# Performance work log

Measured on AMD Instinct MI355X. Metric: run time of the kernel, lower is better.

The kernel has to match this reference:

```python
import jax, jax.numpy as jnp
import numpy as np

H, W = 101, 31
HEADS, DH, FREQ = 8, 64, 64
C_DIM = 256
INNER = HEADS * DH
EPS = 1e-5


def _conv2d(x, w, b):
    # x: (B, Cin, H, W), w: (Cout, Cin, 3, 3) -> SAME padding, stride 1
    y = jax.lax.conv_general_dilated(x, w, (1, 1), 'SAME',
                                     dimension_numbers=('NCHW', 'OIHW', 'NCHW'))
    return y + b[None, :, None, None]


def setup_inputs() -> dict:
    key = jax.random.key(0)
    ks = jax.random.split(key, 8)
    B = 32
    N = H * W  # 3131
    s = 0.02
    x = jax.random.normal(ks[0], (B, N, C_DIM), jnp.float32)
    conv_fx_w = jax.random.normal(ks[1], (INNER, C_DIM, 3, 3), jnp.float32) * s
    conv_fx_b = jnp.zeros((INNER,), jnp.float32)
    conv_x_w = jax.random.normal(ks[2], (INNER, C_DIM, 3, 3), jnp.float32) * s
    conv_x_b = jnp.zeros((INNER,), jnp.float32)
    gate_w = jax.random.normal(ks[3], (FREQ, DH), jnp.float32) * s  # nn.Linear weight (out,in)
    gate_b = jnp.zeros((FREQ,), jnp.float32)
    temperature = jnp.full((1, HEADS, 1, 1), 0.5, jnp.float32)
    ln_gamma = jnp.ones((FREQ, DH), jnp.float32)
    ln_beta = jnp.zeros((FREQ, DH), jnp.float32)
    mlp_w = jax.random.normal(ks[4], (DH, DH), jnp.float32) * s
    out_w = jax.random.normal(ks[5], (C_DIM, INNER), jnp.float32) * s
    out_b = jnp.zeros((C_DIM,), jnp.float32)
    # fixed (non-trainable) spectral basis, L2-normalized per row like F.normalize(dim=-1)
    inver = jax.random.normal(ks[6], (N, FREQ), jnp.float32)
    inver = inver / jnp.linalg.norm(inver, axis=-1, keepdims=True)
    return dict(x=x, conv_fx_w=conv_fx_w, conv_fx_b=conv_fx_b, conv_x_w=conv_x_w,
                conv_x_b=conv_x_b, gate_w=gate_w, gate_b=gate_b,
                temperature=temperature, ln_gamma=ln_gamma, ln_beta=ln_beta,
                mlp_w=mlp_w, out_w=out_w, out_b=out_b, inver=inver)


def reference(x, conv_fx_w, conv_fx_b, conv_x_w, conv_x_b, gate_w, gate_b,
              temperature, ln_gamma, ln_beta, mlp_w, out_w, out_b, inver):
    B, N, C = x.shape
    xi = x.reshape(B, H, W, C).transpose(0, 3, 1, 2)  # (B, C, H, W)

    def proj(w, b):
        y = _conv2d(xi, w, b)                                  # (B, inner, H, W)
        return y.transpose(0, 2, 3, 1).reshape(B, N, HEADS, DH).transpose(0, 2, 1, 3)  # (B,h,N,d)

    fx_mid = proj(conv_fx_w, conv_fx_b)
    x_mid = proj(conv_x_w, conv_x_b)

    temp = jnp.clip(temperature, 0.1, 5.0)                      # (1,h,1,1)
    logits = jnp.einsum('bhnc,gc->bhng', x_mid, gate_w) + gate_b
    gate = jax.nn.softmax(logits / temp, axis=-1)               # (B,h,N,g)
    eigens = gate * inver[None, None]                           # (B,h,N,g)

    spec = jnp.einsum('bhnc,bhng->bhgc', fx_mid, eigens)        # (B,h,g,c)
    # LayerNorm over the trailing (g, c) axes jointly
    mu = spec.mean(axis=(-2, -1), keepdims=True)
    var = spec.var(axis=(-2, -1), keepdims=True)
    spec = (spec - mu) * jax.lax.rsqrt(var + EPS) * ln_gamma + ln_beta

    out_spec = jnp.einsum('bhgi,io->bhgo', spec, mlp_w)
    out_x = jnp.einsum('bhgc,bhng->bhnc', out_spec, eigens)     # (B,h,N,c)
    out_x = out_x.transpose(0, 2, 1, 3).reshape(B, N, HEADS * DH)
    return jnp.einsum('bnd,cd->bnc', out_x, out_w) + out_b      # to_out (dropout is identity)
```

## Files before the change

### kernel.cpp

```cpp
#include <hip/hip_runtime.h>
#include <hip/hip_bf16.h>
#include <stdint.h>

#define HH 101
#define WW 31
#define NN 3131
#define NPAD 3136
#define BB 32
#define NH 8
#define CDIM 256
#define GG 64
#define HP 103
#define WP 33

typedef __attribute__((ext_vector_type(8))) short bf16x8;
typedef __attribute__((ext_vector_type(4))) float f32x4;
typedef __attribute__((ext_vector_type(4))) unsigned short ushort4_t;
typedef __attribute__((ext_vector_type(8))) unsigned short ushort8_t;
typedef __attribute__((ext_vector_type(4))) float float4_t;

static __device__ __forceinline__ unsigned short f2bf(float f) {
  union { float f; uint32_t u; } v; v.f = f;
  uint32_t u = v.u;
  return (unsigned short)((u + 0x7fffu + ((u >> 16) & 1u)) >> 16);
}
static __device__ __forceinline__ float bf2f(unsigned short h) {
  union { uint32_t u; float f; } v; v.u = ((uint32_t)h) << 16;
  return v.f;
}
static __device__ __forceinline__ void gload_lds16(const void* g, void* l) {
  __builtin_amdgcn_global_load_lds((const __attribute__((address_space(1))) void*)g,
                                   (__attribute__((address_space(3))) void*)l, 16, 0, 0);
}
static __device__ __forceinline__ int xcd_swz(int bid, int nwg) {
  int q = nwg >> 3, r = nwg & 7;
  int xcd = bid & 7, pos = bid >> 3;
  int base = (xcd < r) ? xcd * (q + 1) : r * (q + 1) + (xcd - r) * q;
  return base + pos;
}

__global__ void k_pad(const float* __restrict__ x, unsigned short* __restrict__ xpad, int b0) {
  const int xx = blockIdx.x, yy = blockIdx.y, b = blockIdx.z;
  const int t = threadIdx.x;
  ushort4_t o; o.x = 0; o.y = 0; o.z = 0; o.w = 0;
  if (yy >= 1 && yy <= HH && xx >= 1 && xx <= WW) {
    const int n = (yy - 1) * WW + (xx - 1);
    const float4_t v = *(const float4_t*)(x + (((int64_t)(b0 + b) * NN + n) * CDIM + t * 4));
    o.x = f2bf(v.x); o.y = f2bf(v.y); o.z = f2bf(v.z); o.w = f2bf(v.w);
  }
  *(ushort4_t*)(xpad + (((int64_t)b * HP + yy) * WP + xx) * CDIM + t * 4) = o;
}

__global__ void k_wpack(const float* __restrict__ fxw, const float* __restrict__ xw,
                        const float* __restrict__ fxb, const float* __restrict__ xb,
                        const float* __restrict__ gw,
                        unsigned short* __restrict__ Wb, float* __restrict__ bias,
                        unsigned short* __restrict__ gwb) {
  int tid = blockIdx.x * blockDim.x + threadIdx.x;
  const int total = 9 * 1024 * 256;
  if (tid < total) {
    int cin = tid & 255; int rest = tid >> 8; int co = rest & 1023; int t = rest >> 10;
    float v = (co < 512) ? fxw[(int64_t)co * 2304 + cin * 9 + t]
                         : xw[(int64_t)(co - 512) * 2304 + cin * 9 + t];
    Wb[tid] = f2bf(v);
  }
  if (tid < 1024) bias[tid] = (tid < 512) ? fxb[tid] : xb[tid - 512];
  if (tid < 4096) gwb[tid] = f2bf(gw[tid]);
}

__global__ void k_pprep(const float* __restrict__ mlp, const float* __restrict__ outw,
                        unsigned short* __restrict__ Pt) {
  int h = blockIdx.x >> 6, i = blockIdx.x & 63, co = threadIdx.x;
  float a = 0.f;
  for (int c = 0; c < 64; ++c) a += mlp[i * 64 + c] * outw[(int64_t)co * 512 + h * 64 + c];
  Pt[((int64_t)h * 256 + co) * 64 + i] = f2bf(a);
}

__global__ void k_padzero(unsigned short* __restrict__ fxT, unsigned short* __restrict__ xmid,
                          int CB) {
  int tid = blockIdx.x * blockDim.x + threadIdx.x;
  if (tid >= CB * 2560) return;
  {
    int j = tid % 5; int rc = tid / 5;
    fxT[(int64_t)rc * NPAD + NN + j] = 0;
  }
  {
    int d = tid & 63; int rest = tid >> 6;
    int j = rest % 5; int bh = rest / 5;
    xmid[((int64_t)bh * NPAD + NN + j) * 64 + d] = 0;
  }
}

__launch_bounds__(512, 2)
__global__ void k_conv8(const unsigned short* __restrict__ xpad,
                        const unsigned short* __restrict__ Wb,
                        const float* __restrict__ bias,
                        unsigned short* __restrict__ fxT,
                        unsigned short* __restrict__ xmid) {
  extern __shared__ unsigned short lds[];
  const int swz = xcd_swz(blockIdx.x, gridDim.x);
  const int r   = swz % 52;
  const int b   = swz / 52;
  const int bx  = r & 3;
  const int mt  = r >> 2;
  const int tid = threadIdx.x, wid = tid >> 6, lane = tid & 63;
  const int wm = wid & 3, wn = wid >> 2;
  const int arow = lane & 15, col16 = lane >> 4;
  const int n00 = mt * 256, co00 = bx * 256;

  const int srow = wid * 16 + (lane >> 2);
  const int tc   = ((lane & 3) ^ ((lane >> 3) & 3)) * 8;
  int na0 = n00 + srow;        if (na0 >= NN) na0 = NN - 1;
  int na1 = n00 + srow + 128;  if (na1 >= NN) na1 = NN - 1;
  const int y0 = na0 / WW, x0v = na0 % WW;
  const int y1 = na1 / WW, x1v = na1 % WW;
  const unsigned short* aS0 = xpad + ((int64_t)(b * HP + y0) * WP + x0v) * CDIM + tc;
  const unsigned short* aS1 = xpad + ((int64_t)(b * HP + y1) * WP + x1v) * CDIM + tc;
  const unsigned short* bS0 = Wb + (int64_t)(co00 + srow) * CDIM + tc;
  const unsigned short* bS1 = Wb + (int64_t)(co00 + srow + 128) * CDIM + tc;

  const int rdsz = (col16 ^ ((arow >> 1) & 3)) * 8;

  f32x4 acc[4][8] = {};
  bf16x8 a0[4], a1[4], b03[4], b47[4];

#define STAGE_A(s, kk, aoffv)                                        \
  { unsigned short* d = lds + (s) * 32768 + (kk) * 8192 + wid * 512; \
    gload_lds16(aS0 + (aoffv) + (kk) * 32, d);                       \
    gload_lds16(aS1 + (aoffv) + (kk) * 32, d + 4096); }
#define STAGE_B(s, kk, boffv)                                                \
  { unsigned short* d = lds + (s) * 32768 + 16384 + (kk) * 8192 + wid * 512; \
    gload_lds16(bS0 + (boffv) + (kk) * 32, d);                               \
    gload_lds16(bS1 + (boffv) + (kk) * 32, d + 4096); }
#define KOFF(ks, aoffv, boffv)                              \
  { const int tap = (ks) >> 2;                              \
    const int dy = (tap >= 6) + (tap >= 3);                 \
    const int dx = tap - dy * 3;                            \
    const int cb = ((ks) & 3) << 6;                         \
    aoffv = (dy * WP + dx) * CDIM + cb;                     \
    boffv = tap * 262144 + cb; }
#define RD_A(dst, s, kk, mf)                                                             \
  dst = *(const bf16x8*)(lds + (s) * 32768 + (kk) * 8192 +                               \
                         (wm * 64 + (mf) * 16 + arow) * 32 + rdsz);
#define RD_B(dst, s, kk, nf)                                                             \
  dst = *(const bf16x8*)(lds + (s) * 32768 + 16384 + (kk) * 8192 +                       \
                         (wn * 128 + (nf) * 16 + arow) * 32 + rdsz);
#define MFMA16(aset, bset, nbase)                                                        \
  __builtin_amdgcn_s_setprio(1);                                                         \
  _Pragma("unroll")                                                                      \
  for (int mf = 0; mf < 4; ++mf) {                                                       \
    _Pragma("unroll")                                                                    \
    for (int nf = 0; nf < 4; ++nf)                                                       \
      acc[mf][(nbase) + nf] =                                                            \
        __builtin_amdgcn_mfma_f32_16x16x32_bf16(aset[mf], bset[nf], acc[mf][(nbase) + nf], 0, 0, 0); \
  }                                                                                      \
  __builtin_amdgcn_s_setprio(0);

  int aoff0, boff0;
  KOFF(0, aoff0, boff0);
  STAGE_A(0, 0, aoff0); STAGE_B(0, 0, boff0);
  STAGE_A(0, 1, aoff0); STAGE_B(0, 1, boff0);
  asm volatile("s_waitcnt vmcnt(4)" ::: "memory");
  __builtin_amdgcn_s_barrier();
  asm volatile("" ::: "memory");
  #pragma unroll
  for (int i = 0; i < 4; ++i) { RD_A(a0[i], 0, 0, i); }
  #pragma unroll
  for (int i = 0; i < 4; ++i) { RD_B(b03[i], 0, 0, i); }

  #pragma unroll 1
  for (int t = 0; t < 36; ++t) {
    const int cur = t & 1, nxt = cur ^ 1;
    const int tn = (t < 35) ? t + 1 : 35;
    int aoffn, boffn;
    KOFF(tn, aoffn, boffn);

    #pragma unroll
    for (int i = 0; i < 4; ++i) { RD_B(b47[i], cur, 0, 4 + i); }
    STAGE_A(nxt, 0, aoffn);
    asm volatile("s_waitcnt lgkmcnt(4)" ::: "memory");
    __builtin_amdgcn_sched_barrier(0);
    MFMA16(a0, b03, 0);

    STAGE_B(nxt, 0, boffn);
    asm volatile("s_waitcnt vmcnt(4)" ::: "memory");
    __builtin_amdgcn_s_barrier();
    asm volatile("" ::: "memory");
    #pragma unroll
    for (int i = 0; i < 4; ++i) { RD_A(a1[i], cur, 1, i); }
    #pragma unroll
    for (int i = 0; i < 4; ++i) { RD_B(b03[i], cur, 1, i); }
    asm volatile("s_waitcnt lgkmcnt(8)" ::: "memory");
    __builtin_amdgcn_sched_barrier(0);
    MFMA16(a0, b47, 4);

    #pragma unroll
    for (int i = 0; i < 4; ++i) { RD_B(b47[i], cur, 1, 4 + i); }
    STAGE_A(nxt, 1, aoffn);
    asm volatile("s_waitcnt lgkmcnt(4)" ::: "memory");
    __builtin_amdgcn_sched_barrier(0);
    MFMA16(a1, b03, 0);

    STAGE_B(nxt, 1, boffn);
    asm volatile("s_waitcnt vmcnt(4)" ::: "memory");
    __builtin_amdgcn_s_barrier();
    asm volatile("" ::: "memory");
    #pragma unroll
    for (int i = 0; i < 4; ++i) { RD_A(a0[i], nxt, 0, i); }
    #pragma unroll
    for (int i = 0; i < 4; ++i) { RD_B(b03[i], nxt, 0, i); }
    asm volatile("s_waitcnt lgkmcnt(8)" ::: "memory");
    __builtin_amdgcn_sched_barrier(0);
    MFMA16(a1, b47, 4);
  }

  asm volatile("s_waitcnt vmcnt(0) lgkmcnt(0)" ::: "memory");

  const int rowoff = col16 * 4;
  #pragma unroll
  for (int mf = 0; mf < 4; ++mf) {
    const int nr = n00 + wm * 64 + mf * 16 + rowoff;
    #pragma unroll
    for (int nf = 0; nf < 8; ++nf) {
      const int co = co00 + wn * 128 + nf * 16 + arow;
      const float bvs = bias[co];
      const float v0 = acc[mf][nf][0] + bvs;
      const float v1 = acc[mf][nf][1] + bvs;
      const float v2 = acc[mf][nf][2] + bvs;
      const float v3 = acc[mf][nf][3] + bvs;
      if (bx < 2) {
        const int h = co >> 6, c = co & 63;
        unsigned short* dst = fxT + ((int64_t)((b * NH + h) * 64 + c)) * NPAD + nr;
        if (nr + 3 < NN) {
          ushort4_t o; o.x = f2bf(v0); o.y = f2bf(v1); o.z = f2bf(v2); o.w = f2bf(v3);
          *(ushort4_t*)dst = o;
        } else {
          if (nr + 0 < NN) dst[0] = f2bf(v0);
          if (nr + 1 < NN) dst[1] = f2bf(v1);
          if (nr + 2 < NN) dst[2] = f2bf(v2);
          if (nr + 3 < NN) dst[3] = f2bf(v3);
        }
      } else {
        const int h = (co >> 6) & 7, d = co & 63;
        unsigned short* dst = xmid + ((int64_t)(b * NH + h) * NPAD + nr) * 64 + d;
        if (nr + 0 < NN) dst[0] = f2bf(v0);
        if (nr + 1 < NN) dst[64] = f2bf(v1);
        if (nr + 2 < NN) dst[128] = f2bf(v2);
        if (nr + 3 < NN) dst[192] = f2bf(v3);
      }
    }
  }
#undef STAGE_A
#undef STAGE_B
#undef KOFF
#undef RD_A
#undef RD_B
#undef MFMA16
}

__global__ void k_eig(const unsigned short* __restrict__ xmid,
                      const unsigned short* __restrict__ gwb,
                      const float* __restrict__ gateb,
                      const float* __restrict__ temperature,
                      const float* __restrict__ inver,
                      unsigned short* __restrict__ eigT,
                      unsigned short* __restrict__ eigN) {
  __shared__ unsigned short egN[64 * 72];
  __shared__ unsigned short egT[64 * 72];
  const int nt = blockIdx.x, h = blockIdx.y, b = blockIdx.z;
  const int tid = threadIdx.x;
  const int w = tid >> 6, lane = tid & 63;
  const int n0 = nt * 64 + w * 16;
  const int bh = b * NH + h;
  float tv = temperature[h];
  tv = fminf(fmaxf(tv, 0.1f), 5.0f);
  const float itemp = 1.0f / tv;
  const int arow = lane & 15;
  const int koff = (lane >> 4) * 8;
  const unsigned short* aptr = xmid + ((int64_t)bh * NPAD + (n0 + arow)) * 64 + koff;
  bf16x8 a0 = *(const bf16x8*)(aptr);
  bf16x8 a1 = *(const bf16x8*)(aptr + 32);
  f32x4 acc[4] = {};
  #pragma unroll
  for (int ng = 0; ng < 4; ++ng) {
    const unsigned short* bptr = gwb + (ng * 16 + arow) * 64 + koff;
    bf16x8 b0 = *(const bf16x8*)(bptr);
    bf16x8 b1 = *(const bf16x8*)(bptr + 32);
    acc[ng] = __builtin_amdgcn_mfma_f32_16x16x32_bf16(a0, b0, acc[ng], 0, 0, 0);
    acc[ng] = __builtin_amdgcn_mfma_f32_16x16x32_bf16(a1, b1, acc[ng], 0, 0, 0);
  }
  #pragma unroll
  for (int r = 0; r < 4; ++r) {
    const int nl = w * 16 + ((lane >> 4) << 2) + r;
    const int n = nt * 64 + nl;
    float vals[4];
    #pragma unroll
    for (int ng = 0; ng < 4; ++ng) vals[ng] = (acc[ng][r] + gateb[ng * 16 + arow]) * itemp;
    float mx = fmaxf(fmaxf(vals[0], vals[1]), fmaxf(vals[2], vals[3]));
    #pragma unroll
    for (int s = 1; s < 16; s <<= 1) mx = fmaxf(mx, __shfl_xor(mx, s));
    float ex[4]; float sum = 0.f;
    #pragma unroll
    for (int ng = 0; ng < 4; ++ng) { ex[ng] = __expf(vals[ng] - mx); sum += ex[ng]; }
    #pragma unroll
    for (int s = 1; s < 16; s <<= 1) sum += __shfl_xor(sum, s);
    const float inv = 1.0f / sum;
    const bool valid = (n < NN);
    #pragma unroll
    for (int ng = 0; ng < 4; ++ng) {
      const int g = ng * 16 + arow;
      float iv = valid ? inver[(int64_t)n * GG + g] : 0.f;
      unsigned short u = valid ? f2bf(ex[ng] * inv * iv) : (unsigned short)0;
      egN[nl * 72 + g] = u;
      egT[g * 72 + nl] = u;
    }
  }
  __syncthreads();
  const int row = tid >> 2, c0 = (tid & 3) << 4;
  {
    ushort8_t v0 = *(ushort8_t*)&egN[row * 72 + c0];
    ushort8_t v1 = *(ushort8_t*)&egN[row * 72 + c0 + 8];
    unsigned short* dst = eigN + ((int64_t)bh * NPAD + nt * 64 + row) * 64 + c0;
    *(ushort8_t*)dst = v0; *(ushort8_t*)(dst + 8) = v1;
  }
  {
    ushort8_t v0 = *(ushort8_t*)&egT[row * 72 + c0];
    ushort8_t v1 = *(ushort8_t*)&egT[row * 72 + c0 + 8];
    unsigned short* dst = eigT + ((int64_t)(bh * 64 + row)) * NPAD + nt * 64 + c0;
    *(ushort8_t*)dst = v0; *(ushort8_t*)(dst + 8) = v1;
  }
}

__global__ void k_specA(const unsigned short* __restrict__ eigT,
                        const unsigned short* __restrict__ fxT,
                        float* __restrict__ part) {
  const int q = blockIdx.x, bhl = blockIdx.y;
  const int tid = threadIdx.x, w = tid >> 6, lane = tid & 63;
  const int s = q * 4 + w;
  const int ks0 = (98 * s) >> 3, ks1 = (98 * (s + 1)) >> 3;
  const int arow = lane & 15, col16 = lane >> 4;
  const int koff = col16 * 8;
  const unsigned short* eb = eigT + (int64_t)bhl * 64 * NPAD;
  const unsigned short* fb = fxT + (int64_t)bhl * 64 * NPAD;
  f32x4 acc[4][4] = {};
  for (int ks = ks0; ks < ks1; ++ks) {
    const int k0 = ks * 32 + koff;
    bf16x8 av[4], bv[4];
    #pragma unroll
    for (int mg = 0; mg < 4; ++mg) av[mg] = *(const bf16x8*)(eb + (int64_t)(mg * 16 + arow) * NPAD + k0);
    #pragma unroll
    for (int ng = 0; ng < 4; ++ng) bv[ng] = *(const bf16x8*)(fb + (int64_t)(ng * 16 + arow) * NPAD + k0);
    #pragma unroll
    for (int mg = 0; mg < 4; ++mg)
      #pragma unroll
      for (int ng = 0; ng < 4; ++ng)
        acc[mg][ng] = __builtin_amdgcn_mfma_f32_16x16x32_bf16(av[mg], bv[ng], acc[mg][ng], 0, 0, 0);
  }
  float* pb = part + ((int64_t)bhl * 8 + s) * 4096;
  #pragma unroll
  for (int mg = 0; mg < 4; ++mg)
    #pragma unroll
    for (int ng = 0; ng < 4; ++ng)
      #pragma unroll
      for (int r = 0; r < 4; ++r)
        pb[(mg * 16 + col16 * 4 + r) * 64 + ng * 16 + arow] = acc[mg][ng][r];
}

__global__ void k_specB(const float* __restrict__ part,
                        const float* __restrict__ gamma, const float* __restrict__ beta,
                        const unsigned short* __restrict__ Pt,
                        unsigned short* __restrict__ m2t) {
  __shared__ unsigned short specb[64 * 64];
  __shared__ float red[8];
  __shared__ unsigned short mstrip[4 * 64 * 72];
  const int bhl = blockIdx.x;
  const int h = bhl & 7, bl = bhl >> 3;
  const int tid = threadIdx.x, w = tid >> 6, lane = tid & 63;
  const int arow = lane & 15, col16 = lane >> 4;
  const int koff = col16 * 8;
  const float* pb = part + (int64_t)bhl * 8 * 4096;

  float vloc[16];
  float lsum = 0.f, lsq = 0.f;
  #pragma unroll
  for (int idx = 0; idx < 16; ++idx) {
    const int e = tid + idx * 256;
    float v = 0.f;
    #pragma unroll
    for (int s = 0; s < 8; ++s) v += pb[s * 4096 + e];
    vloc[idx] = v; lsum += v; lsq += v * v;
  }
  #pragma unroll
  for (int s = 1; s < 64; s <<= 1) { lsum += __shfl_xor(lsum, s); lsq += __shfl_xor(lsq, s); }
  if (lane == 0) { red[w] = lsum; red[4 + w] = lsq; }
  __syncthreads();
  const float tsum = red[0] + red[1] + red[2] + red[3];
  const float tsq = red[4] + red[5] + red[6] + red[7];
  const float mu = tsum * (1.0f / 4096.0f);
  const float var = tsq * (1.0f / 4096.0f) - mu * mu;
  const float rs = rsqrtf(var + 1e-5f);
  #pragma unroll
  for (int idx = 0; idx < 16; ++idx) {
    const int e = tid + idx * 256;
    const int g = e >> 6, c = e & 63;
    float sv = (vloc[idx] - mu) * rs * gamma[e] + beta[e];
    specb[g * 64 + ((((c >> 3) ^ (g & 7))) << 3) + (c & 7)] = f2bf(sv);
  }
  __syncthreads();

  f32x4 a2[4][4] = {};
  const unsigned short* pth = Pt + ((int64_t)h * 256 + w * 64) * 64;
  #pragma unroll
  for (int kk = 0; kk < 2; ++kk) {
    const int i0 = kk * 32 + koff;
    const int i8 = (i0 >> 3);
    bf16x8 av2[4], bv2[4];
    #pragma unroll
    for (int mg = 0; mg < 4; ++mg) {
      const int g = mg * 16 + arow;
      av2[mg] = *(const bf16x8*)(specb + g * 64 + ((i8 ^ (g & 7)) << 3));
    }
    #pragma unroll
    for (int ng = 0; ng < 4; ++ng)
      bv2[ng] = *(const bf16x8*)(pth + (ng * 16 + arow) * 64 + i0);
    #pragma unroll
    for (int mg = 0; mg < 4; ++mg)
      #pragma unroll
      for (int ng = 0; ng < 4; ++ng)
        a2[mg][ng] = __builtin_amdgcn_mfma_f32_16x16x32_bf16(av2[mg], bv2[ng], a2[mg][ng], 0, 0, 0);
  }
  unsigned short* ms = mstrip + w * (64 * 72);
  #pragma unroll
  for (int mg = 0; mg < 4; ++mg)
    #pragma unroll
    for (int ng = 0; ng < 4; ++ng)
      #pragma unroll
      for (int r = 0; r < 4; ++r)
        ms[(ng * 16 + arow) * 72 + mg * 16 + col16 * 4 + r] = f2bf(a2[mg][ng][r]);
  __syncthreads();
  #pragma unroll
  for (int e0 = 0; e0 < 8; ++e0) {
    const int e = lane + e0 * 64;
    const int row = e >> 3, g8 = e & 7;
    ushort8_t v = *(ushort8_t*)&ms[row * 72 + g8 * 8];
    *(ushort8_t*)(m2t + ((int64_t)(bl * 256 + w * 64 + row)) * 512 + h * 64 + g8 * 8) = v;
  }
}

__launch_bounds__(256)
__global__ void k_out(const unsigned short* __restrict__ eigN,
                      const unsigned short* __restrict__ m2t,
                      const float* __restrict__ outb,
                      float* __restrict__ out, int b0) {
  const int swz = xcd_swz(blockIdx.x, gridDim.x);
  const int ct = swz & 1;
  const int mt = (swz >> 1) % 25;
  const int b  = swz / 50;
  const int w = threadIdx.x >> 6, lane = threadIdx.x & 63;
  const int wm = w >> 1, wn = w & 1;
  const int arow = lane & 15, koff = (lane >> 4) * 8;
  const int co0 = ct * 128 + wn * 64;
  const int n0 = mt * 128 + wm * 64;
  f32x4 acc[4][4] = {};
  const unsigned short* ebase = eigN + (int64_t)b * NH * NPAD * 64;
  const unsigned short* mbase = m2t + (int64_t)b * 256 * 512;
  for (int ks = 0; ks < 16; ++ks) {
    const int hh = ks >> 1;
    const int g0 = (ks & 1) * 32 + koff;
    bf16x8 av[4], bv[4];
    #pragma unroll
    for (int mg = 0; mg < 4; ++mg) {
      int n = n0 + mg * 16 + arow;
      if (n > NPAD - 1) n = NPAD - 1;
      av[mg] = *(const bf16x8*)(ebase + ((int64_t)hh * NPAD + n) * 64 + g0);
    }
    #pragma unroll
    for (int ng = 0; ng < 4; ++ng)
      bv[ng] = *(const bf16x8*)(mbase + (int64_t)(co0 + ng * 16 + arow) * 512 + ks * 32 + koff);
    #pragma unroll
    for (int mg = 0; mg < 4; ++mg)
      #pragma unroll
      for (int ng = 0; ng < 4; ++ng)
        acc[mg][ng] = __builtin_amdgcn_mfma_f32_16x16x32_bf16(av[mg], bv[ng], acc[mg][ng], 0, 0, 0);
  }
  #pragma unroll
  for (int mg = 0; mg < 4; ++mg) {
    const int nr = n0 + mg * 16 + ((lane >> 4) << 2);
    #pragma unroll
    for (int ng = 0; ng < 4; ++ng) {
      const int co = co0 + ng * 16 + arow;
      const float bv = outb[co];
      #pragma unroll
      for (int r = 0; r < 4; ++r) {
        if (nr + r < NN)
          out[((int64_t)(b0 + b) * NN + nr + r) * 256 + co] = acc[mg][ng][r] + bv;
      }
    }
  }
}

extern "C" void kernel_launch(void* const* d_in, const int* in_sizes, int n_in,
                              void* d_out, int out_size, void* d_ws, size_t ws_size,
                              hipStream_t stream) {
  const float* x     = (const float*)d_in[0];
  const float* fxw   = (const float*)d_in[1];
  const float* fxb   = (const float*)d_in[2];
  const float* xw    = (const float*)d_in[3];
  const float* xb    = (const float*)d_in[4];
  const float* gw    = (const float*)d_in[5];
  const float* gb    = (const float*)d_in[6];
  const float* temp  = (const float*)d_in[7];
  const float* gamma = (const float*)d_in[8];
  const float* beta  = (const float*)d_in[9];
  const float* mlp   = (const float*)d_in[10];
  const float* outw  = (const float*)d_in[11];
  const float* outb  = (const float*)d_in[12];
  const float* inver = (const float*)d_in[13];
  float* out = (float*)d_out;
  char* ws = (char*)d_ws;
  (void)in_sizes; (void)n_in; (void)out_size;

  hipFuncSetAttribute(reinterpret_cast<const void*>(k_conv8),
                      hipFuncAttributeMaxDynamicSharedMemorySize, 131072);

  int CB = 1;
  {
    const int cands[5] = {16, 8, 4, 2, 1};
    for (int i = 0; i < 5; ++i) {
      unsigned long long need = 4993024ull + (unsigned long long)cands[i] * 14847488ull;
      if (need <= (unsigned long long)ws_size) { CB = cands[i]; break; }
    }
  }

  unsigned short* Wb   = (unsigned short*)(ws + 0);
  float*          bias = (float*)(ws + 4718592);
  unsigned short* gwb  = (unsigned short*)(ws + 4722688);
  unsigned short* Pt   = (unsigned short*)(ws + 4730880);
  const size_t F0      = 4993024;
  const size_t szXpad  = (size_t)CB * 1740288;
  const size_t szM2t   = (size_t)CB * 262144;
  const size_t szBig   = (size_t)CB * 3211264;
  unsigned short* xpad = (unsigned short*)(ws + F0);
  float*          part = (float*)(ws + F0);
  unsigned short* m2t  = (unsigned short*)(ws + F0 + szXpad);
  unsigned short* fxT  = (unsigned short*)(ws + F0 + szXpad + szM2t);
  unsigned short* xmid = (unsigned short*)(ws + F0 + szXpad + szM2t + szBig);
  unsigned short* eigT = (unsigned short*)(ws + F0 + szXpad + szM2t + 2 * szBig);
  unsigned short* eigN = (unsigned short*)(ws + F0 + szXpad + szM2t + 3 * szBig);

  k_wpack<<<dim3(9216), dim3(256), 0, stream>>>(fxw, xw, fxb, xb, gw, Wb, bias, gwb);
  k_pprep<<<dim3(512), dim3(256), 0, stream>>>(mlp, outw, Pt);

  for (int b0 = 0; b0 < BB; b0 += CB) {
    k_pad<<<dim3(WP, HP, CB), dim3(64), 0, stream>>>(x, xpad, b0);
    k_padzero<<<dim3(CB * 10), dim3(256), 0, stream>>>(fxT, xmid, CB);
    k_conv8<<<dim3(52 * CB), dim3(512), 131072, stream>>>(xpad, Wb, bias, fxT, xmid);
    k_eig<<<dim3(49, 8, CB), dim3(256), 0, stream>>>(xmid, gwb, gb, temp, inver, eigT, eigN);
    k_specA<<<dim3(2, CB * 8), dim3(256), 0, stream>>>(eigT, fxT, part);
    k_specB<<<dim3(CB * 8), dim3(256), 0, stream>>>(part, gamma, beta, Pt, m2t);
    k_out<<<dim3(50 * CB), dim3(256), 0, stream>>>(eigN, m2t, outb, out, b0);
  }
}
```

Baseline: 889.3 us.

## Fuse gate-softmax eigen computation with spectral projection via shared-memory eigT

Merges k_eig and k_specA into one kernel. Each block computes the gated eigen tile for 448 tokens, keeps the transposed copy in LDS and immediately runs the eig^T·fx MFMA reduction, then reduces the four wave partials in shared memory before writing 7 partials per (b,h). This removes the global write and re-read of the eigT buffer and one kernel launch. The costs are large dynamic LDS (about 66 KB, limiting occupancy), serialized wave reductions, and a different grid shape with 7 blocks per (b,h).

```diff
diff --git a/kernel.cpp b/kernel.cpp
--- a/kernel.cpp
+++ b/kernel.cpp
@@ -258,112 +258,119 @@
 #undef MFMA16
 }
 
-__global__ void k_eig(const unsigned short* __restrict__ xmid,
-                      const unsigned short* __restrict__ gwb,
-                      const float* __restrict__ gateb,
-                      const float* __restrict__ temperature,
-                      const float* __restrict__ inver,
-                      unsigned short* __restrict__ eigT,
-                      unsigned short* __restrict__ eigN) {
-  __shared__ unsigned short egN[64 * 72];
-  __shared__ unsigned short egT[64 * 72];
-  const int nt = blockIdx.x, h = blockIdx.y, b = blockIdx.z;
-  const int tid = threadIdx.x;
-  const int w = tid >> 6, lane = tid & 63;
-  const int n0 = nt * 64 + w * 16;
-  const int bh = b * NH + h;
+__launch_bounds__(256, 2)
+__global__ void k_eigspec(const unsigned short* __restrict__ xmid,
+                          const unsigned short* __restrict__ gwb,
+                          const float* __restrict__ gateb,
+                          const float* __restrict__ temperature,
+                          const float* __restrict__ inver,
+                          const unsigned short* __restrict__ fxT,
+                          unsigned short* __restrict__ eigN,
+                          float* __restrict__ part) {
+  extern __shared__ unsigned short sdyn[];
+  unsigned short* egT = sdyn;
+  unsigned short* egN = sdyn + 64 * 456;
+  const int q = blockIdx.x, bhl = blockIdx.y;
+  const int h = bhl & 7;
+  const int tid = threadIdx.x, w = tid >> 6, lane = tid & 63;
+  const int arow = lane & 15, col16 = lane >> 4;
+  const int koff = col16 * 8;
+  const int nbase = q * 448;
   float tv = temperature[h];
   tv = fminf(fmaxf(tv, 0.1f), 5.0f);
   const float itemp = 1.0f / tv;
-  const int arow = lane & 15;
-  const int koff = (lane >> 4) * 8;
-  const unsigned short* aptr = xmid + ((int64_t)bh * NPAD + (n0 + arow)) * 64 + koff;
-  bf16x8 a0 = *(const bf16x8*)(aptr);
-  bf16x8 a1 = *(const bf16x8*)(aptr + 32);
-  f32x4 acc[4] = {};
-  #pragma unroll
-  for (int ng = 0; ng < 4; ++ng) {
-    const unsigned short* bptr = gwb + (ng * 16 + arow) * 64 + koff;
-    bf16x8 b0 = *(const bf16x8*)(bptr);
-    bf16x8 b1 = *(const bf16x8*)(bptr + 32);
-    acc[ng] = __builtin_amdgcn_mfma_f32_16x16x32_bf16(a0, b0, acc[ng], 0, 0, 0);
-    acc[ng] = __builtin_amdgcn_mfma_f32_16x16x32_bf16(a1, b1, acc[ng], 0, 0, 0);
-  }
-  #pragma unroll
-  for (int r = 0; r < 4; ++r) {
-    const int nl = w * 16 + ((lane >> 4) << 2) + r;
-    const int n = nt * 64 + nl;
-    float vals[4];
-    #pragma unroll
-    for (int ng = 0; ng < 4; ++ng) vals[ng] = (acc[ng][r] + gateb[ng * 16 + arow]) * itemp;
-    float mx = fmaxf(fmaxf(vals[0], vals[1]), fmaxf(vals[2], vals[3]));
-    #pragma unroll
-    for (int s = 1; s < 16; s <<= 1) mx = fmaxf(mx, __shfl_xor(mx, s));
-    float ex[4]; float sum = 0.f;
-    #pragma unroll
-    for (int ng = 0; ng < 4; ++ng) { ex[ng] = __expf(vals[ng] - mx); sum += ex[ng]; }
-    #pragma unroll
-    for (int s = 1; s < 16; s <<= 1) sum += __shfl_xor(sum, s);
-    const float inv = 1.0f / sum;
-    const bool valid = (n < NN);
+
+  #pragma unroll 1
+  for (int st = 0; st < 7; ++st) {
+    const int n0 = nbase + st * 64 + w * 16;
+    const unsigned short* aptr = xmid + ((int64_t)bhl * NPAD + (n0 + arow)) * 64 + koff;
+    bf16x8 a0 = *(const bf16x8*)(aptr);
+    bf16x8 a1 = *(const bf16x8*)(aptr + 32);
+    f32x4 acc[4] = {};
     #pragma unroll
     for (int ng = 0; ng < 4; ++ng) {
-      const int g = ng * 16 + arow;
-      float iv = valid ? inver[(int64_t)n * GG + g] : 0.f;
-      unsigned short u = valid ? f2bf(ex[ng] * inv * iv) : (unsigned short)0;
-      egN[nl * 72 + g] = u;
-      egT[g * 72 + nl] = u;
-    }
-  }
-  __syncthreads();
-  const int row = tid >> 2, c0 = (tid & 3) << 4;
-  {
+      const unsigned short* bptr = gwb + (ng * 16 + arow) * 64 + koff;
+      bf16x8 b0 = *(const bf16x8*)(bptr);
+      bf16x8 b1 = *(const bf16x8*)(bptr + 32);
+      acc[ng] = __builtin_amdgcn_mfma_f32_16x16x32_bf16(a0, b0, acc[ng], 0, 0, 0);
+      acc[ng] = __builtin_amdgcn_mfma_f32_16x16x32_bf16(a1, b1, acc[ng], 0, 0, 0);
+    }
+    #pragma unroll
+    for (int r = 0; r < 4; ++r) {
+      const int nl64 = w * 16 + (col16 << 2) + r;
+      const int n = nbase + st * 64 + nl64;
+      float vals[4];
+      #pragma unroll
+      for (int ng = 0; ng < 4; ++ng) vals[ng] = (acc[ng][r] + gateb[ng * 16 + arow]) * itemp;
+      float mx = fmaxf(fmaxf(vals[0], vals[1]), fmaxf(vals[2], vals[3]));
+      #pragma unroll
+      for (int s = 1; s < 16; s <<= 1) mx = fmaxf(mx, __shfl_xor(mx, s));
+      float ex[4]; float sum = 0.f;
+      #pragma unroll
+      for (int ng = 0; ng < 4; ++ng) { ex[ng] = __expf(vals[ng] - mx); sum += ex[ng]; }
+      #pragma unroll
+      for (int s = 1; s < 16; s <<= 1) sum += __shfl_xor(sum, s);
+      const float inv = 1.0f / sum;
+      const bool valid = (n < NN);
+      #pragma unroll
+      for (int ng = 0; ng < 4; ++ng) {
+        const int g = ng * 16 + arow;
+        float iv = valid ? inver[(int64_t)n * GG + g] : 0.f;
+        unsigned short u = valid ? f2bf(ex[ng] * inv * iv) : (unsigned short)0;
+        egN[nl64 * 72 + g] = u;
+        egT[g * 456 + st * 64 + nl64] = u;
+      }
+    }
+    __syncthreads();
+    const int row = tid >> 2, c0 = (tid & 3) << 4;
     ushort8_t v0 = *(ushort8_t*)&egN[row * 72 + c0];
     ushort8_t v1 = *(ushort8_t*)&egN[row * 72 + c0 + 8];
-    unsigned short* dst = eigN + ((int64_t)bh * NPAD + nt * 64 + row) * 64 + c0;
+    unsigned short* dst = eigN + ((int64_t)bhl * NPAD + nbase + st * 64 + row) * 64 + c0;
     *(ushort8_t*)dst = v0; *(ushort8_t*)(dst + 8) = v1;
-  }
+    __syncthreads();
+  }
+
+  const int ks0 = (14 * w) >> 2, ks1 = (14 * (w + 1)) >> 2;
+  f32x4 acc2[4][4] = {};
+  const unsigned short* fb = fxT + (int64_t)bhl * 64 * NPAD + nbase;
+  for (int ks = ks0; ks < ks1; ++ks) {
+    const int kloc = ks * 32 + koff;
+    bf16x8 av[4], bv[4];
+    #pragma unroll
+    for (int mg = 0; mg < 4; ++mg)
+      av[mg] = *(const bf16x8*)(egT + (mg * 16 + arow) * 456 + kloc);
+    #pragma unroll
+    for (int ng = 0; ng < 4; ++ng)
+      bv[ng] = *(const bf16x8*)(fb + (int64_t)(ng * 16 + arow) * NPAD + kloc);
+    #pragma unroll
+    for (int mg = 0; mg < 4; ++mg)
+      #pragma unroll
+      for (int ng = 0; ng < 4; ++ng)
+        acc2[mg][ng] = __builtin_amdgcn_mfma_f32_16x16x32_bf16(av[mg], bv[ng], acc2[mg][ng], 0, 0, 0);
+  }
+  __syncthreads();
+  float* facc = (float*)egT;
   {
-    ushort8_t v0 = *(ushort8_t*)&egT[row * 72 + c0];
-    ushort8_t v1 = *(ushort8_t*)&egT[row * 72 + c0 + 8];
-    unsigned short* dst = eigT + ((int64_t)(bh * 64 + row)) * NPAD + nt * 64 + c0;
-    *(ushort8_t*)dst = v0; *(ushort8_t*)(dst + 8) = v1;
-  }
-}
-
-__global__ void k_specA(const unsigned short* __restrict__ eigT,
-                        const unsigned short* __restrict__ fxT,
-                        float* __restrict__ part) {
-  const int q = blockIdx.x, bhl = blockIdx.y;
-  const int tid = threadIdx.x, w = tid >> 6, lane = tid & 63;
-  const int s = q * 4 + w;
-  const int ks0 = (98 * s) >> 3, ks1 = (98 * (s + 1)) >> 3;
-  const int arow = lane & 15, col16 = lane >> 4;
-  const int koff = col16 * 8;
-  const unsigned short* eb = eigT + (int64_t)bhl * 64 * NPAD;
-  const unsigned short* fb = fxT + (int64_t)bhl * 64 * NPAD;
-  f32x4 acc[4][4] = {};
-  for (int ks = ks0; ks < ks1; ++ks) {
-    const int k0 = ks * 32 + koff;
-    bf16x8 av[4], bv[4];
-    #pragma unroll
-    for (int mg = 0; mg < 4; ++mg) av[mg] = *(const bf16x8*)(eb + (int64_t)(mg * 16 + arow) * NPAD + k0);
-    #pragma unroll
-    for (int ng = 0; ng < 4; ++ng) bv[ng] = *(const bf16x8*)(fb + (int64_t)(ng * 16 + arow) * NPAD + k0);
-    #pragma unroll
-    for (int mg = 0; mg < 4; ++mg)
-      #pragma unroll
-      for (int ng = 0; ng < 4; ++ng)
-        acc[mg][ng] = __builtin_amdgcn_mfma_f32_16x16x32_bf16(av[mg], bv[ng], acc[mg][ng], 0, 0, 0);
-  }
-  float* pb = part + ((int64_t)bhl * 8 + s) * 4096;
-  #pragma unroll
-  for (int mg = 0; mg < 4; ++mg)
-    #pragma unroll
-    for (int ng = 0; ng < 4; ++ng)
-      #pragma unroll
-      for (int r = 0; r < 4; ++r)
-        pb[(mg * 16 + col16 * 4 + r) * 64 + ng * 16 + arow] = acc[mg][ng][r];
+    float* strip = (float*)egT;
+    for (int ww = 0; ww < 4; ++ww) {
+      if (w == ww) {
+        #pragma unroll
+        for (int mg = 0; mg < 4; ++mg)
+          #pragma unroll
+          for (int ng = 0; ng < 4; ++ng)
+            #pragma unroll
+            for (int r = 0; r < 4; ++r) {
+              const int g = mg * 16 + col16 * 4 + r, c = ng * 16 + arow;
+              if (ww == 0) strip[g * 65 + c] = acc2[mg][ng][r];
+              else         strip[g * 65 + c] += acc2[mg][ng][r];
+            }
+      }
+      __syncthreads();
+    }
+    float* pb = part + ((int64_t)bhl * 7 + q) * 4096;
+    for (int e = tid; e < 4096; e += 256)
+      pb[e] = strip[(e >> 6) * 65 + (e & 63)];
+  }
 }
 
 __global__ void k_specB(const float* __restrict__ part,
@@ -378,7 +385,7 @@
   const int tid = threadIdx.x, w = tid >> 6, lane = tid & 63;
   const int arow = lane & 15, col16 = lane >> 4;
   const int koff = col16 * 8;
-  const float* pb = part + (int64_t)bhl * 8 * 4096;
+  const float* pb = part + (int64_t)bhl * 7 * 4096;
 
   float vloc[16];
   float lsum = 0.f, lsq = 0.f;
@@ -387,7 +394,7 @@
     const int e = tid + idx * 256;
     float v = 0.f;
     #pragma unroll
-    for (int s = 0; s < 8; ++s) v += pb[s * 4096 + e];
+    for (int s = 0; s < 7; ++s) v += pb[s * 4096 + e];
     vloc[idx] = v; lsum += v; lsq += v * v;
   }
   #pragma unroll
@@ -522,6 +529,8 @@
 
   hipFuncSetAttribute(reinterpret_cast<const void*>(k_conv8),
                       hipFuncAttributeMaxDynamicSharedMemorySize, 131072);
+  hipFuncSetAttribute(reinterpret_cast<const void*>(k_eigspec),
+                      hipFuncAttributeMaxDynamicSharedMemorySize, 67584);
 
   int CB = 1;
   {
@@ -545,8 +554,7 @@
   unsigned short* m2t  = (unsigned short*)(ws + F0 + szXpad);
   unsigned short* fxT  = (unsigned short*)(ws + F0 + szXpad + szM2t);
   unsigned short* xmid = (unsigned short*)(ws + F0 + szXpad + szM2t + szBig);
-  unsigned short* eigT = (unsigned short*)(ws + F0 + szXpad + szM2t + 2 * szBig);
-  unsigned short* eigN = (unsigned short*)(ws + F0 + szXpad + szM2t + 3 * szBig);
+  unsigned short* eigN = (unsigned short*)(ws + F0 + szXpad + szM2t + 2 * szBig);
 
   k_wpack<<<dim3(9216), dim3(256), 0, stream>>>(fxw, xw, fxb, xb, gw, Wb, bias, gwb);
   k_pprep<<<dim3(512), dim3(256), 0, stream>>>(mlp, outw, Pt);
@@ -555,8 +563,8 @@
     k_pad<<<dim3(WP, HP, CB), dim3(64), 0, stream>>>(x, xpad, b0);
     k_padzero<<<dim3(CB * 10), dim3(256), 0, stream>>>(fxT, xmid, CB);
     k_conv8<<<dim3(52 * CB), dim3(512), 131072, stream>>>(xpad, Wb, bias, fxT, xmid);
-    k_eig<<<dim3(49, 8, CB), dim3(256), 0, stream>>>(xmid, gwb, gb, temp, inver, eigT, eigN);
-    k_specA<<<dim3(2, CB * 8), dim3(256), 0, stream>>>(eigT, fxT, part);
+    k_eigspec<<<dim3(7, CB * 8), dim3(256), 67584, stream>>>(xmid, gwb, gb, temp, inver,
+                                                             fxT, eigN, part);
     k_specB<<<dim3(CB * 8), dim3(256), 0, stream>>>(part, gamma, beta, Pt, m2t);
     k_out<<<dim3(50 * CB), dim3(256), 0, stream>>>(eigN, m2t, outb, out, b0);
   }
```

Result: slower. 911.6 us (+2.5%).
